# Performance work log

Measured on AMD Instinct MI355X. Metric: run time of the kernel, lower is better.

The kernel has to match this reference:

```python
import jax, jax.numpy as jnp
import numpy as np

B, N, D, H = 4, 4096, 512, 512
EDGE_P = 0.01  # adjacency density


def _glorot(key, shape):
    fan_in, fan_out = shape
    limit = np.sqrt(6.0 / (fan_in + fan_out)).astype(np.float32)
    return jax.random.uniform(key, shape, jnp.float32, -limit, limit)


def setup_inputs() -> dict:
    key = jax.random.key(0)
    ks = jax.random.split(key, 9)
    batch_graph = jax.random.normal(ks[0], (B, N, D), jnp.float32)
    adj = (jax.random.uniform(ks[1], (B, N, N)) < EDGE_P).astype(jnp.float32)
    adj = jnp.minimum(adj + jnp.eye(N, dtype=jnp.float32)[None], 1.0)  # self loops, 0/1
    return {
        "batch_graph": batch_graph,
        "adj": adj,
        "W1": _glorot(ks[2], (D, H)), "b1": jnp.zeros((H,), jnp.float32),
        "W2": _glorot(ks[3], (H, H)), "b2": jnp.zeros((H,), jnp.float32),
        "W3": _glorot(ks[4], (H, D)), "b3": jnp.zeros((D,), jnp.float32),
    }


def _normalize_adj(adj):
    # Faithful to GCN.normalize_sparse_adj: D^{-1/2} A^T D^{-1/2}
    rowsum = adj.sum(axis=1)                       # [B, N] (sum over dim 1, as in torch)
    d_inv_sqrt = jnp.where(rowsum > 0, jax.lax.rsqrt(jnp.maximum(rowsum, 1e-30)), 0.0)
    # (A @ diag(d))^T @ diag(d)  ->  d_i * A[j,i] * d_j
    return d_inv_sqrt[:, :, None] * jnp.swapaxes(adj, 1, 2) * d_inv_sqrt[:, None, :]


def reference(batch_graph, adj, W1, b1, W2, b2, W3, b3):
    # Block-diagonal big_adj @ big_graph == independent per-batch matmuls;
    # we exploit that instead of materializing the [B*N, B*N] dense matrix.
    a = _normalize_adj(adj)                                   # [B, N, N]
    # GraphConvolution (pygcn-style): out = adj @ (x @ W) + b; dropout = identity (eval)
    h = jax.nn.relu(jnp.einsum('bij,bjd->bid', a, batch_graph @ W1) + b1)
    h = jax.nn.relu(jnp.einsum('bij,bjd->bid', a, h @ W2) + b2)
    out = jnp.einsum('bij,bjd->bid', a, h @ W3) + b3          # [B, N, D]
    return out
```

## Files before the change

### kernel.cpp

```cpp
#include <hip/hip_runtime.h>
#include <stdint.h>

#define CAP 128
#define RPB 4

typedef __attribute__((ext_vector_type(8))) short bf16x8;
typedef __attribute__((ext_vector_type(4))) float f32x4;

typedef __attribute__((address_space(3))) uint32_t lds_u32;
typedef __attribute__((address_space(1))) const uint32_t glb_u32;

__device__ __forceinline__ unsigned short f2bf(float f) {
  union { float f; uint32_t u; } c; c.f = f;
  return (unsigned short)((c.u + 0x7fffu + ((c.u >> 16) & 1u)) >> 16);
}
__device__ __forceinline__ float bf2f(uint32_t b) {
  union { uint32_t u; float f; } c; c.u = b << 16; return c.f;
}
__device__ __forceinline__ float as_f32(uint32_t u) {
  union { uint32_t u; float f; } c; c.u = u; return c.f;
}

__global__ __launch_bounds__(256) void k_detect(const uint32_t* __restrict__ a,
                                                int* __restrict__ flag) {
  int i = blockIdx.x * 256 + threadIdx.x;
  bool found = false;
  for (int k = 0; k < 64; k++) {
    uint32_t x = a[(size_t)k * 65536 + i];
    if (x == 0x00003F80u || x == 0x3F803F80u) found = true;
  }
  if (found) flag[0] = 1;
}

__global__ __launch_bounds__(256) void k_build(const void* __restrict__ adjp,
                                               int* __restrict__ cnt,
                                               int* __restrict__ cols,
                                               const int* __restrict__ flag) {
  int gid = blockIdx.x * 256 + threadIdx.x;
  if (flag[0]) {
    const uint4* a = (const uint4*)adjp;
    uint4 v = a[gid];
    int i0 = (gid & 511) * 8;
    int j  = (gid >> 9) & 4095;
    int b  = gid >> 21;
    int base = b << 12;
    uint32_t w[4] = {v.x, v.y, v.z, v.w};
#pragma unroll
    for (int q = 0; q < 4; q++) {
      if (w[q] & 0xffffu) {
        int c = base + i0 + q * 2;
        int p = atomicAdd(&cnt[c], 1);
        if (p < CAP) cols[(size_t)c * CAP + p] = j;
      }
      if (w[q] >> 16) {
        int c = base + i0 + q * 2 + 1;
        int p = atomicAdd(&cnt[c], 1);
        if (p < CAP) cols[(size_t)c * CAP + p] = j;
      }
    }
  } else {
    const float4* a = (const float4*)adjp;
#pragma unroll
    for (int it = 0; it < 2; it++) {
      int v4 = gid + it * 8388608;
      float4 v = a[v4];
      int i0 = (v4 & 1023) * 4;
      int j  = (v4 >> 10) & 4095;
      int b  = v4 >> 22;
      int base = b << 12;
      float e[4] = {v.x, v.y, v.z, v.w};
#pragma unroll
      for (int q = 0; q < 4; q++) {
        if (e[q] != 0.0f) {
          int c = base + i0 + q;
          int p = atomicAdd(&cnt[c], 1);
          if (p < CAP) cols[(size_t)c * CAP + p] = j;
        }
      }
    }
  }
}

__global__ __launch_bounds__(256) void k_prep(const int* __restrict__ cnt,
                                              float* __restrict__ dinv,
                                              const void* b1, const void* b2,
                                              const void* b3,
                                              float* __restrict__ b1f,
                                              float* __restrict__ b2f,
                                              float* __restrict__ b3f,
                                              const int* __restrict__ flag) {
  int id = blockIdx.x * 256 + threadIdx.x;
  if (id < 16384) {
    int c = cnt[id];
    dinv[id] = (c > 0) ? 1.0f / sqrtf((float)c) : 0.0f;
  } else {
    int o = id - 16384;
    if (o < 1536) {
      const void* src = (o < 512) ? b1 : (o < 1024) ? b2 : b3;
      float* dst = (o < 512) ? b1f : (o < 1024) ? b2f : b3f;
      int i = o & 511;
      dst[i] = flag[0] ? bf2f(((const ushort*)src)[i]) : ((const float*)src)[i];
    }
  }
}

__global__ __launch_bounds__(256) void k_convx(const void* __restrict__ xp,
                                               ushort* __restrict__ xb,
                                               const int* __restrict__ flag) {
  int gid = blockIdx.x * 256 + threadIdx.x;
  if (flag[0]) {
    const uint4* in = (const uint4*)xp;
    ((uint4*)xb)[gid] = in[gid];
  } else {
    const float4* in = (const float4*)xp;
#pragma unroll
    for (int it = 0; it < 2; it++) {
      int i = gid + it * 1048576;
      float4 v = in[i];
      uint32_t lo = (uint32_t)f2bf(v.x) | ((uint32_t)f2bf(v.y) << 16);
      uint32_t hi = (uint32_t)f2bf(v.z) | ((uint32_t)f2bf(v.w) << 16);
      ((uint2*)xb)[i] = make_uint2(lo, hi);
    }
  }
}

__global__ __launch_bounds__(256) void k_wconv(const void* w1, const void* w2,
                                               const void* w3,
                                               ushort* __restrict__ wt1,
                                               ushort* __restrict__ wt2,
                                               ushort* __restrict__ wt3,
                                               const int* __restrict__ flag) {
  int id = blockIdx.x * 256 + threadIdx.x;
  int w = id >> 18;
  int o = id & 262143;
  const void* wp = (w == 0) ? w1 : (w == 1) ? w2 : w3;
  ushort* wt = (w == 0) ? wt1 : (w == 1) ? wt2 : wt3;
  int n = o >> 9, k = o & 511;
  if (flag[0]) wt[o] = ((const ushort*)wp)[k * 512 + n];
  else         wt[o] = f2bf(((const float*)wp)[k * 512 + n]);
}

__device__ __forceinline__ void gl_lds16(const ushort* g, ushort* l) {
  __builtin_amdgcn_global_load_lds((glb_u32*)g, (lds_u32*)l, 16, 0, 0);
}

__global__ __launch_bounds__(256) void k_gemm(const ushort* __restrict__ X,
                                              const ushort* __restrict__ WT,
                                              ushort* __restrict__ Z) {
  __shared__ ushort As[128 * 32];
  __shared__ ushort Bs[128 * 32];
  const int K = 512, NO = 512;
  int tid = threadIdx.x;
  int m0 = blockIdx.y * 128, n0 = blockIdx.x * 128;
  int lane = tid & 63;
  int wv = tid >> 6;
  int wm = (wv >> 1) << 6;
  int wn = (wv & 1) << 6;
  int lr = lane & 15;
  int lq = lane >> 4;

  f32x4 zero = {0.f, 0.f, 0.f, 0.f};
  f32x4 acc[4][4];
#pragma unroll
  for (int im = 0; im < 4; im++)
#pragma unroll
    for (int in_ = 0; in_ < 4; in_++) acc[im][in_] = zero;

  const ushort* Xg = X  + (size_t)(m0 + (tid >> 2)) * K + ((tid & 3) << 3);
  const ushort* Wg = WT + (size_t)(n0 + (tid >> 2)) * K + ((tid & 3) << 3);

  for (int kt = 0; kt < K; kt += 32) {
    __syncthreads();
    gl_lds16(Xg + kt,                    &As[tid * 8]);
    gl_lds16(Xg + kt + (size_t)64 * K,   &As[2048 + tid * 8]);
    gl_lds16(Wg + kt,                    &Bs[tid * 8]);
    gl_lds16(Wg + kt + (size_t)64 * K,   &Bs[2048 + tid * 8]);
    __syncthreads();
    bf16x8 af[4], bfr[4];
#pragma unroll
    for (int im = 0; im < 4; im++)
      af[im] = *(const bf16x8*)&As[(wm + im * 16 + lr) * 32 + lq * 8];
#pragma unroll
    for (int in_ = 0; in_ < 4; in_++)
      bfr[in_] = *(const bf16x8*)&Bs[(wn + in_ * 16 + lr) * 32 + lq * 8];
#pragma unroll
    for (int im = 0; im < 4; im++)
#pragma unroll
      for (int in_ = 0; in_ < 4; in_++)
        acc[im][in_] = __builtin_amdgcn_mfma_f32_16x16x32_bf16(
            af[im], bfr[in_], acc[im][in_], 0, 0, 0);
  }

#pragma unroll
  for (int im = 0; im < 4; im++) {
    int row0 = m0 + wm + im * 16 + lq * 4;
#pragma unroll
    for (int in_ = 0; in_ < 4; in_++) {
      int col = n0 + wn + in_ * 16 + lr;
#pragma unroll
      for (int r = 0; r < 4; r++)
        Z[(size_t)(row0 + r) * NO + col] = f2bf(acc[im][in_][r]);
    }
  }
}

__global__ __launch_bounds__(256) void k_spmm(const ushort* __restrict__ Z,
                                              const int* __restrict__ cnt,
                                              const int* __restrict__ cols,
                                              const float* __restrict__ dinv,
                                              const float* __restrict__ bias,
                                              void* __restrict__ outp,
                                              int do_relu, int is_final,
                                              const int* __restrict__ flag) {
  __shared__ int   sj[RPB][CAP];
  __shared__ float sv[RPB][CAP];
  int B = blockIdx.x;
  int wv = threadIdx.x >> 6;
  int lane = threadIdx.x & 63;
  int batch = (B & 7) >> 1;
  int lb = ((B >> 3) << 1) | (B & 1);
  int r = (batch << 12) + lb * RPB + wv;
  int base = batch << 12;

  int nnz = cnt[r];
  if (nnz > CAP) nnz = CAP;
  float dr = dinv[r];
  for (int k = lane; k < nnz; k += 64) {
    int j = cols[(size_t)r * CAP + k];
    sj[wv][k] = j;
    sv[wv][k] = dr * dinv[base + j];
  }

  const ushort* Zb = Z + (size_t)base * 512 + lane * 8;
  const float4* bp = (const float4*)bias + lane * 2;
  float4 bb0 = bp[0], bb1 = bp[1];
  float a[8] = {bb0.x, bb0.y, bb0.z, bb0.w, bb1.x, bb1.y, bb1.z, bb1.w};

  int k = 0;
  for (; k + 2 <= nnz; k += 2) {
    int j0 = sj[wv][k], j1 = sj[wv][k + 1];
    float v0 = sv[wv][k], v1 = sv[wv][k + 1];
    uint4 z0 = *(const uint4*)(Zb + (size_t)j0 * 512);
    uint4 z1 = *(const uint4*)(Zb + (size_t)j1 * 512);
    uint32_t w0[4] = {z0.x, z0.y, z0.z, z0.w};
    uint32_t w1[4] = {z1.x, z1.y, z1.z, z1.w};
#pragma unroll
    for (int q = 0; q < 4; q++) {
      a[q * 2]     += v0 * as_f32(w0[q] << 16);
      a[q * 2 + 1] += v0 * as_f32(w0[q] & 0xffff0000u);
      a[q * 2]     += v1 * as_f32(w1[q] << 16);
      a[q * 2 + 1] += v1 * as_f32(w1[q] & 0xffff0000u);
    }
  }
  if (k < nnz) {
    int j0 = sj[wv][k];
    float v0 = sv[wv][k];
    uint4 z0 = *(const uint4*)(Zb + (size_t)j0 * 512);
    uint32_t w0[4] = {z0.x, z0.y, z0.z, z0.w};
#pragma unroll
    for (int q = 0; q < 4; q++) {
      a[q * 2]     += v0 * as_f32(w0[q] << 16);
      a[q * 2 + 1] += v0 * as_f32(w0[q] & 0xffff0000u);
    }
  }

  if (do_relu) {
#pragma unroll
    for (int q = 0; q < 8; q++) a[q] = fmaxf(a[q], 0.f);
  }

  if (!is_final || flag[0]) {
    uint4 o;
    o.x = (uint32_t)f2bf(a[0]) | ((uint32_t)f2bf(a[1]) << 16);
    o.y = (uint32_t)f2bf(a[2]) | ((uint32_t)f2bf(a[3]) << 16);
    o.z = (uint32_t)f2bf(a[4]) | ((uint32_t)f2bf(a[5]) << 16);
    o.w = (uint32_t)f2bf(a[6]) | ((uint32_t)f2bf(a[7]) << 16);
    *(uint4*)((ushort*)outp + (size_t)r * 512 + lane * 8) = o;
  } else {
    float4 o0 = make_float4(a[0], a[1], a[2], a[3]);
    float4 o1 = make_float4(a[4], a[5], a[6], a[7]);
    float4* op = (float4*)((float*)outp + (size_t)r * 512 + lane * 8);
    op[0] = o0; op[1] = o1;
  }
}

extern "C" void kernel_launch(void* const* d_in, const int* in_sizes, int n_in,
                              void* d_out, int out_size, void* d_ws, size_t ws_size,
                              hipStream_t stream) {
  const void* X  = d_in[0];
  const void* A  = d_in[1];
  const void* W1 = d_in[2]; const void* b1 = d_in[3];
  const void* W2 = d_in[4]; const void* b2 = d_in[5];
  const void* W3 = d_in[6]; const void* b3 = d_in[7];

  char* ws = (char*)d_ws;
  size_t off = 0;
  auto alloc = [&](size_t bytes) -> void* {
    void* p = ws + off;
    off += (bytes + 255) & ~(size_t)255;
    return p;
  };
  int*    cnt  = (int*)alloc(16384 * 4);
  int*    flag = (int*)alloc(4);
  float*  dinv = (float*)alloc(16384 * 4);
  int*    cols = (int*)alloc((size_t)16384 * CAP * 4);
  ushort* W1T  = (ushort*)alloc(512 * 512 * 2);
  ushort* W2T  = (ushort*)alloc(512 * 512 * 2);
  ushort* W3T  = (ushort*)alloc(512 * 512 * 2);
  float*  b1f  = (float*)alloc(512 * 4);
  float*  b2f  = (float*)alloc(512 * 4);
  float*  b3f  = (float*)alloc(512 * 4);
  ushort* Xb   = (ushort*)alloc((size_t)16384 * 512 * 2);
  ushort* Zb   = (ushort*)alloc((size_t)16384 * 512 * 2);
  ushort* Hb   = (ushort*)alloc((size_t)16384 * 512 * 2);

  hipMemsetAsync(cnt, 0, 65536 + 256, stream);

  k_detect<<<256, 256, 0, stream>>>((const uint32_t*)A, flag);
  k_build<<<32768, 256, 0, stream>>>(A, cnt, cols, flag);
  k_prep<<<70, 256, 0, stream>>>(cnt, dinv, b1, b2, b3, b1f, b2f, b3f, flag);
  k_convx<<<4096, 256, 0, stream>>>(X, Xb, flag);
  k_wconv<<<3072, 256, 0, stream>>>(W1, W2, W3, W1T, W2T, W3T, flag);

  dim3 gg(4, 128);
  k_gemm<<<gg, 256, 0, stream>>>(Xb, W1T, Zb);
  k_spmm<<<4096, 256, 0, stream>>>(Zb, cnt, cols, dinv, b1f, Hb, 1, 0, flag);
  k_gemm<<<gg, 256, 0, stream>>>(Hb, W2T, Zb);
  k_spmm<<<4096, 256, 0, stream>>>(Zb, cnt, cols, dinv, b2f, Xb, 1, 0, flag);
  k_gemm<<<gg, 256, 0, stream>>>(Xb, W3T, Zb);
  k_spmm<<<4096, 256, 0, stream>>>(Zb, cnt, cols, dinv, b3f, d_out, 0, 1, flag);
}
```

Measured before the change: 600.0 us.

## Remap GEMM/SpMM blocks per XCD, split SpMM columns, add nontemporal streaming loads

The GEMM grid becomes 1D, and tiles are remapped so that each XCD (blockIdx mod 8) works on a contiguous band of M rows for one batch with two N tiles, improving L2 locality. SpMM now launches twice as many blocks. Each block handles half the feature columns (4 per lane instead of 8), and batches are mapped to XCD pairs so each XCD's L2 holds one batch's Z. Streaming reads of the dense adjacency, X and the cols array, plus output stores, use nontemporal hints to avoid polluting the cache. The trade-off is that SpMM repeats the neighbor-list gather and LDS setup twice per row and uses narrower 8-byte loads.

```diff
diff --git a/kernel.cpp b/kernel.cpp
--- a/kernel.cpp
+++ b/kernel.cpp
@@ -6,6 +6,8 @@
 
 typedef __attribute__((ext_vector_type(8))) short bf16x8;
 typedef __attribute__((ext_vector_type(4))) float f32x4;
+typedef __attribute__((ext_vector_type(4))) uint32_t u32x4;
+typedef __attribute__((ext_vector_type(2))) uint32_t u32x2;
 
 typedef __attribute__((address_space(3))) uint32_t lds_u32;
 typedef __attribute__((address_space(1))) const uint32_t glb_u32;
@@ -26,7 +28,7 @@
   int i = blockIdx.x * 256 + threadIdx.x;
   bool found = false;
   for (int k = 0; k < 64; k++) {
-    uint32_t x = a[(size_t)k * 65536 + i];
+    uint32_t x = __builtin_nontemporal_load(&a[(size_t)k * 65536 + i]);
     if (x == 0x00003F80u || x == 0x3F803F80u) found = true;
   }
   if (found) flag[0] = 1;
@@ -38,13 +40,13 @@
                                                const int* __restrict__ flag) {
   int gid = blockIdx.x * 256 + threadIdx.x;
   if (flag[0]) {
-    const uint4* a = (const uint4*)adjp;
-    uint4 v = a[gid];
+    const u32x4* a = (const u32x4*)adjp;
+    u32x4 v = __builtin_nontemporal_load(&a[gid]);
     int i0 = (gid & 511) * 8;
     int j  = (gid >> 9) & 4095;
     int b  = gid >> 21;
     int base = b << 12;
-    uint32_t w[4] = {v.x, v.y, v.z, v.w};
+    uint32_t w[4] = {v[0], v[1], v[2], v[3]};
 #pragma unroll
     for (int q = 0; q < 4; q++) {
       if (w[q] & 0xffffu) {
@@ -59,16 +61,16 @@
       }
     }
   } else {
-    const float4* a = (const float4*)adjp;
+    const f32x4* a = (const f32x4*)adjp;
 #pragma unroll
     for (int it = 0; it < 2; it++) {
       int v4 = gid + it * 8388608;
-      float4 v = a[v4];
+      f32x4 v = __builtin_nontemporal_load(&a[v4]);
       int i0 = (v4 & 1023) * 4;
       int j  = (v4 >> 10) & 4095;
       int b  = v4 >> 22;
       int base = b << 12;
-      float e[4] = {v.x, v.y, v.z, v.w};
+      float e[4] = {v[0], v[1], v[2], v[3]};
 #pragma unroll
       for (int q = 0; q < 4; q++) {
         if (e[q] != 0.0f) {
@@ -109,16 +111,17 @@
                                                const int* __restrict__ flag) {
   int gid = blockIdx.x * 256 + threadIdx.x;
   if (flag[0]) {
-    const uint4* in = (const uint4*)xp;
-    ((uint4*)xb)[gid] = in[gid];
+    const u32x4* in = (const u32x4*)xp;
+    u32x4 v = __builtin_nontemporal_load(&in[gid]);
+    ((u32x4*)xb)[gid] = v;
   } else {
-    const float4* in = (const float4*)xp;
+    const f32x4* in = (const f32x4*)xp;
 #pragma unroll
     for (int it = 0; it < 2; it++) {
       int i = gid + it * 1048576;
-      float4 v = in[i];
-      uint32_t lo = (uint32_t)f2bf(v.x) | ((uint32_t)f2bf(v.y) << 16);
-      uint32_t hi = (uint32_t)f2bf(v.z) | ((uint32_t)f2bf(v.w) << 16);
+      f32x4 v = __builtin_nontemporal_load(&in[i]);
+      uint32_t lo = (uint32_t)f2bf(v[0]) | ((uint32_t)f2bf(v[1]) << 16);
+      uint32_t hi = (uint32_t)f2bf(v[2]) | ((uint32_t)f2bf(v[3]) << 16);
       ((uint2*)xb)[i] = make_uint2(lo, hi);
     }
   }
@@ -151,7 +154,11 @@
   __shared__ ushort Bs[128 * 32];
   const int K = 512, NO = 512;
   int tid = threadIdx.x;
-  int m0 = blockIdx.y * 128, n0 = blockIdx.x * 128;
+  int l = blockIdx.x;
+  int xcd = l & 7, idx = l >> 3;
+  int mt = ((xcd >> 1) << 5) + (idx >> 1);
+  int ntile = ((xcd & 1) << 1) + (idx & 1);
+  int m0 = mt << 7, n0 = ntile << 7;
   int lane = tid & 63;
   int wv = tid >> 6;
   int wm = (wv >> 1) << 6;
@@ -214,11 +221,12 @@
                                               const int* __restrict__ flag) {
   __shared__ int   sj[RPB][CAP];
   __shared__ float sv[RPB][CAP];
-  int B = blockIdx.x;
+  int Bk = blockIdx.x;
   int wv = threadIdx.x >> 6;
   int lane = threadIdx.x & 63;
-  int batch = (B & 7) >> 1;
-  int lb = ((B >> 3) << 1) | (B & 1);
+  int batch = (Bk & 7) >> 1;
+  int half  = Bk & 1;
+  int lb    = Bk >> 3;
   int r = (batch << 12) + lb * RPB + wv;
   int base = batch << 12;
 
@@ -226,61 +234,48 @@
   if (nnz > CAP) nnz = CAP;
   float dr = dinv[r];
   for (int k = lane; k < nnz; k += 64) {
-    int j = cols[(size_t)r * CAP + k];
+    int j = __builtin_nontemporal_load(&cols[(size_t)r * CAP + k]);
     sj[wv][k] = j;
     sv[wv][k] = dr * dinv[base + j];
   }
 
-  const ushort* Zb = Z + (size_t)base * 512 + lane * 8;
-  const float4* bp = (const float4*)bias + lane * 2;
-  float4 bb0 = bp[0], bb1 = bp[1];
-  float a[8] = {bb0.x, bb0.y, bb0.z, bb0.w, bb1.x, bb1.y, bb1.z, bb1.w};
+  int c0 = (half << 8) + (lane << 2);
+  const ushort* Zb = Z + (size_t)base * 512 + c0;
+  f32x4 bb = *(const f32x4*)(bias + c0);
+  float a0 = bb[0], a1 = bb[1], a2 = bb[2], a3 = bb[3];
 
   int k = 0;
   for (; k + 2 <= nnz; k += 2) {
     int j0 = sj[wv][k], j1 = sj[wv][k + 1];
     float v0 = sv[wv][k], v1 = sv[wv][k + 1];
-    uint4 z0 = *(const uint4*)(Zb + (size_t)j0 * 512);
-    uint4 z1 = *(const uint4*)(Zb + (size_t)j1 * 512);
-    uint32_t w0[4] = {z0.x, z0.y, z0.z, z0.w};
-    uint32_t w1[4] = {z1.x, z1.y, z1.z, z1.w};
-#pragma unroll
-    for (int q = 0; q < 4; q++) {
-      a[q * 2]     += v0 * as_f32(w0[q] << 16);
-      a[q * 2 + 1] += v0 * as_f32(w0[q] & 0xffff0000u);
-      a[q * 2]     += v1 * as_f32(w1[q] << 16);
-      a[q * 2 + 1] += v1 * as_f32(w1[q] & 0xffff0000u);
-    }
+    u32x2 z0 = *(const u32x2*)(Zb + (size_t)j0 * 512);
+    u32x2 z1 = *(const u32x2*)(Zb + (size_t)j1 * 512);
+    a0 += v0 * as_f32(z0[0] << 16); a1 += v0 * as_f32(z0[0] & 0xffff0000u);
+    a2 += v0 * as_f32(z0[1] << 16); a3 += v0 * as_f32(z0[1] & 0xffff0000u);
+    a0 += v1 * as_f32(z1[0] << 16); a1 += v1 * as_f32(z1[0] & 0xffff0000u);
+    a2 += v1 * as_f32(z1[1] << 16); a3 += v1 * as_f32(z1[1] & 0xffff0000u);
   }
   if (k < nnz) {
     int j0 = sj[wv][k];
     float v0 = sv[wv][k];
-    uint4 z0 = *(const uint4*)(Zb + (size_t)j0 * 512);
-    uint32_t w0[4] = {z0.x, z0.y, z0.z, z0.w};
-#pragma unroll
-    for (int q = 0; q < 4; q++) {
-      a[q * 2]     += v0 * as_f32(w0[q] << 16);
-      a[q * 2 + 1] += v0 * as_f32(w0[q] & 0xffff0000u);
-    }
+    u32x2 z0 = *(const u32x2*)(Zb + (size_t)j0 * 512);
+    a0 += v0 * as_f32(z0[0] << 16); a1 += v0 * as_f32(z0[0] & 0xffff0000u);
+    a2 += v0 * as_f32(z0[1] << 16); a3 += v0 * as_f32(z0[1] & 0xffff0000u);
   }
 
   if (do_relu) {
-#pragma unroll
-    for (int q = 0; q < 8; q++) a[q] = fmaxf(a[q], 0.f);
+    a0 = fmaxf(a0, 0.f); a1 = fmaxf(a1, 0.f);
+    a2 = fmaxf(a2, 0.f); a3 = fmaxf(a3, 0.f);
   }
 
   if (!is_final || flag[0]) {
-    uint4 o;
-    o.x = (uint32_t)f2bf(a[0]) | ((uint32_t)f2bf(a[1]) << 16);
-    o.y = (uint32_t)f2bf(a[2]) | ((uint32_t)f2bf(a[3]) << 16);
-    o.z = (uint32_t)f2bf(a[4]) | ((uint32_t)f2bf(a[5]) << 16);
-    o.w = (uint32_t)f2bf(a[6]) | ((uint32_t)f2bf(a[7]) << 16);
-    *(uint4*)((ushort*)outp + (size_t)r * 512 + lane * 8) = o;
+    u32x2 o;
+    o[0] = (uint32_t)f2bf(a0) | ((uint32_t)f2bf(a1) << 16);
+    o[1] = (uint32_t)f2bf(a2) | ((uint32_t)f2bf(a3) << 16);
+    __builtin_nontemporal_store(o, (u32x2*)((ushort*)outp + (size_t)r * 512 + c0));
   } else {
-    float4 o0 = make_float4(a[0], a[1], a[2], a[3]);
-    float4 o1 = make_float4(a[4], a[5], a[6], a[7]);
-    float4* op = (float4*)((float*)outp + (size_t)r * 512 + lane * 8);
-    op[0] = o0; op[1] = o1;
+    f32x4 o = {a0, a1, a2, a3};
+    __builtin_nontemporal_store(o, (f32x4*)((float*)outp + (size_t)r * 512 + c0));
   }
 }
 
@@ -322,11 +317,10 @@
   k_convx<<<4096, 256, 0, stream>>>(X, Xb, flag);
   k_wconv<<<3072, 256, 0, stream>>>(W1, W2, W3, W1T, W2T, W3T, flag);
 
-  dim3 gg(4, 128);
-  k_gemm<<<gg, 256, 0, stream>>>(Xb, W1T, Zb);
-  k_spmm<<<4096, 256, 0, stream>>>(Zb, cnt, cols, dinv, b1f, Hb, 1, 0, flag);
-  k_gemm<<<gg, 256, 0, stream>>>(Hb, W2T, Zb);
-  k_spmm<<<4096, 256, 0, stream>>>(Zb, cnt, cols, dinv, b2f, Xb, 1, 0, flag);
-  k_gemm<<<gg, 256, 0, stream>>>(Xb, W3T, Zb);
-  k_spmm<<<4096, 256, 0, stream>>>(Zb, cnt, cols, dinv, b3f, d_out, 0, 1, flag);
-}
+  k_gemm<<<512, 256, 0, stream>>>(Xb, W1T, Zb);
+  k_spmm<<<8192, 256, 0, stream>>>(Zb, cnt, cols, dinv, b1f, Hb, 1, 0, flag);
+  k_gemm<<<512, 256, 0, stream>>>(Hb, W2T, Zb);
+  k_spmm<<<8192, 256, 0, stream>>>(Zb, cnt, cols, dinv, b2f, Xb, 1, 0, flag);
+  k_gemm<<<512, 256, 0, stream>>>(Xb, W3T, Zb);
+  k_spmm<<<8192, 256, 0, stream>>>(Zb, cnt, cols, dinv, b3f, d_out, 0, 1, flag);
+}
```

Measured after the change: 655.4 us. +9.2%, slower.
